# Kernel optimization log

Measured on AMD Instinct MI355X. Metric: run time of the kernel, lower is better.

The kernel has to match this reference:

```python
import jax, jax.numpy as jnp
import numpy as np

NEG_INF = -1e30


def setup_inputs() -> dict:
    key = jax.random.key(0)
    ks = jax.random.split(key, 8)
    B, N, I, O, H = 8, 1024, 64, 32, 4
    return {
        "x": jax.random.normal(ks[0], (B, N, I), dtype=jnp.float32),
        "adj": jax.random.randint(ks[1], (N, N), 0, 2, dtype=jnp.int32),
        "source_prior": jax.random.normal(ks[2], (B, N), dtype=jnp.float32),
        "beta": jax.random.normal(ks[3], (H,), dtype=jnp.float32),
        "weight": jax.random.normal(ks[4], (H, I, O), dtype=jnp.float32) * (1.0 / np.sqrt(I)),
        "attn_src": jax.random.normal(ks[5], (H, O), dtype=jnp.float32) * (1.0 / np.sqrt(O)),
        "attn_dst": jax.random.normal(ks[6], (H, O), dtype=jnp.float32) * (1.0 / np.sqrt(O)),
        "bias": jnp.zeros((H, O), dtype=jnp.float32),
    }


def reference(x, adj, source_prior, beta, weight, attn_src, attn_dst, bias):
    B, N, _ = x.shape
    H, _, O = weight.shape
    # Per-head projection + bias: [B,H,N,O]
    projected = jnp.einsum('bni,hio->bhno', x, weight) + bias[None, :, None, :]
    src_scores = jnp.einsum('bhnd,hd->bhn', projected, attn_src)  # [B,H,N]
    dst_scores = jnp.einsum('bhnd,hd->bhn', projected, attn_dst)  # [B,H,N]
    # Additive attention logits: [B,H,dst,src]
    logits = jax.nn.leaky_relu(dst_scores[..., :, None] + src_scores[..., None, :],
                               negative_slope=0.2)
    # Source-prior correction
    gain = jax.nn.softplus(beta).reshape(1, H, 1, 1)
    logits = logits + gain * source_prior[:, None, None, :]
    # Masked softmax over sources; fully-masked rows stay zero
    mask = (adj != 0)[None, None, :, :]  # [1,1,N,N]
    masked = jnp.where(mask, logits, NEG_INF)
    row_max = jnp.max(masked, axis=-1, keepdims=True)
    row_max = jnp.where(jnp.isfinite(row_max) & (row_max > NEG_INF / 2),
                        row_max, jnp.zeros_like(row_max))
    exp_logits = jnp.where(mask, jnp.exp(logits - row_max), 0.0)
    eps = jnp.finfo(logits.dtype).eps
    denom = jnp.maximum(jnp.sum(exp_logits, axis=-1, keepdims=True), eps)
    attention = exp_logits / denom  # [B,H,N,N]
    # Weighted aggregation: [B,H,N,O]
    output = jnp.einsum('bhij,bhjd->bhid', attention, projected)
    # concat=True: [B,N,H*O]
    encoded = jnp.transpose(output, (0, 2, 1, 3)).reshape(B, N, H * O)
    return encoded
```

## Files before the change

kernel.cpp:

```cpp
#include <hip/hip_runtime.h>
#include <math.h>

#define NB 8
#define NN 1024
#define NI 64
#define NO 32
#define NH 4
#define NEGINF (-1e30f)

typedef _Float16 half8 __attribute__((ext_vector_type(8)));
typedef _Float16 half4v __attribute__((ext_vector_type(4)));
typedef float floatx4 __attribute__((ext_vector_type(4)));

__global__ __launch_bounds__(256) void k_pack(const int* __restrict__ adj,
                                              unsigned char* __restrict__ adjb) {
    const int i = blockIdx.x * 256 + threadIdx.x;
    const int4 v = ((const int4*)adj)[i];
    unsigned int p = (v.x ? 1u : 0u) | ((v.y ? 1u : 0u) << 8) |
                     ((v.z ? 1u : 0u) << 16) | ((v.w ? 1u : 0u) << 24);
    ((unsigned int*)adjb)[i] = p;
}

__global__ __launch_bounds__(256) void k_proj(
    const float* __restrict__ x, const float* __restrict__ beta,
    const float* __restrict__ weight, const float* __restrict__ attn_src,
    const float* __restrict__ attn_dst, const float* __restrict__ bias,
    const float* __restrict__ prior,
    _Float16* __restrict__ projT,
    float* __restrict__ src_s, float* __restrict__ dst_s, float* __restrict__ gp)
{
    __shared__ __align__(16) float xs[32 * 64];
    __shared__ __align__(16) float ws[4 * 64 * 36];
    const int t = threadIdx.x;
    const int ntile = blockIdx.x, b = blockIdx.y;
    const int n0b = ntile * 32;
    {
        const float4* xsrc = (const float4*)(x + ((size_t)b * NN + n0b) * NI);
        float4* xd = (float4*)xs;
        xd[t] = xsrc[t];
        xd[t + 256] = xsrc[t + 256];
    }
    #pragma unroll
    for (int k = 0; k < 8; ++k) {
        int e = t + k * 256;
        int h = e >> 9, rem = e & 511, i = rem >> 3, o4 = rem & 7;
        float4 wv = *(const float4*)(weight + (h * NI + i) * NO + o4 * 4);
        *(float4*)&ws[h * 2304 + i * 36 + o4 * 4] = wv;
    }
    __syncthreads();

    const int o4 = t & 7, h = (t >> 3) & 3, ng = t >> 5;
    const int o0 = o4 * 4, nl0 = ng * 4;
    float acc[4][4];
    #pragma unroll
    for (int kn = 0; kn < 4; ++kn)
        #pragma unroll
        for (int oo = 0; oo < 4; ++oo) acc[kn][oo] = 0.f;

    for (int i = 0; i < NI; ++i) {
        const float4 wv = *(const float4*)&ws[h * 2304 + i * 36 + o0];
        #pragma unroll
        for (int kn = 0; kn < 4; ++kn) {
            const float xv = xs[(nl0 + kn) * 64 + i];
            acc[kn][0] = fmaf(xv, wv.x, acc[kn][0]);
            acc[kn][1] = fmaf(xv, wv.y, acc[kn][1]);
            acc[kn][2] = fmaf(xv, wv.z, acc[kn][2]);
            acc[kn][3] = fmaf(xv, wv.w, acc[kn][3]);
        }
    }
    const float4 bv  = *(const float4*)(bias + h * NO + o0);
    const float4 asv = *(const float4*)(attn_src + h * NO + o0);
    const float4 adv = *(const float4*)(attn_dst + h * NO + o0);
    const int bh = b * NH + h;
    float ssum[4], dsum[4];
    #pragma unroll
    for (int kn = 0; kn < 4; ++kn) {
        acc[kn][0] += bv.x; acc[kn][1] += bv.y;
        acc[kn][2] += bv.z; acc[kn][3] += bv.w;
        ssum[kn] = acc[kn][0]*asv.x + acc[kn][1]*asv.y + acc[kn][2]*asv.z + acc[kn][3]*asv.w;
        dsum[kn] = acc[kn][0]*adv.x + acc[kn][1]*adv.y + acc[kn][2]*adv.z + acc[kn][3]*adv.w;
    }
    #pragma unroll
    for (int oo = 0; oo < 4; ++oo) {
        half4v hv;
        hv[0] = (_Float16)acc[0][oo]; hv[1] = (_Float16)acc[1][oo];
        hv[2] = (_Float16)acc[2][oo]; hv[3] = (_Float16)acc[3][oo];
        *(half4v*)(projT + ((size_t)(bh * NO + o0 + oo)) * NN + n0b + nl0) = hv;
    }
    #pragma unroll
    for (int msk = 1; msk <= 4; msk <<= 1) {
        #pragma unroll
        for (int kn = 0; kn < 4; ++kn) {
            ssum[kn] += __shfl_xor(ssum[kn], msk, 64);
            dsum[kn] += __shfl_xor(dsum[kn], msk, 64);
        }
    }
    if (o4 == 0) {
        const float bx = beta[h];
        const float sp = fmaxf(bx, 0.f) + log1pf(__expf(-fabsf(bx)));
        #pragma unroll
        for (int kn = 0; kn < 4; ++kn) {
            const int n = n0b + nl0 + kn;
            src_s[bh * NN + n] = ssum[kn];
            dst_s[bh * NN + n] = dsum[kn];
            gp[bh * NN + n] = sp * prior[b * NN + n];
        }
    }
}

#define SPH 512
#define SP  520

__global__ __launch_bounds__(256) void k_attn(
    const unsigned char* __restrict__ adjb,
    const _Float16* __restrict__ projT,
    const float* __restrict__ src_s, const float* __restrict__ dst_s,
    const float* __restrict__ gp,
    float* __restrict__ out)
{
    __shared__ __align__(16) _Float16 vt[NO * SP];
    __shared__ __align__(16) float srcs[NN];
    __shared__ __align__(16) float gps[NN];
    const int t = threadIdx.x;
    const int lane = t & 63, wave = t >> 6;
    const int dtile = blockIdx.x, h = blockIdx.y, b = blockIdx.z;
    const int bh = b * NH + h;
    {
        ((float4*)srcs)[t] = ((const float4*)(src_s + bh * NN))[t];
        ((float4*)gps)[t]  = ((const float4*)(gp + bh * NN))[t];
    }
    const int m = lane & 15, quad = lane >> 4;
    const int d = dtile * 64 + wave * 16 + m;
    const float dreg = dst_s[bh * NN + d];
    const unsigned char* adjr = adjb + (size_t)d * NN;
    const _Float16* ptrow = projT + (size_t)bh * NO * NN;

    floatx4 acc0 = {0.f, 0.f, 0.f, 0.f}, acc1 = {0.f, 0.f, 0.f, 0.f};
    float m_s = NEGINF, l_s = 0.f;
    uint2 apre = *(const uint2*)(adjr + quad * 8);

    for (int ph = 0; ph < 2; ++ph) {
        #pragma unroll
        for (int rr = 0; rr < 8; ++rr) {
            const int o = wave * 8 + rr;
            *(half8*)&vt[o * SP + lane * 8] =
                *(const half8*)(ptrow + (size_t)o * NN + ph * SPH + lane * 8);
        }
        __syncthreads();
        for (int st = 0; st < 16; ++st) {
            const int gs = ph * 16 + st;
            const uint2 acur = apre;
            if (gs < 31) apre = *(const uint2*)(adjr + (gs + 1) * 32 + quad * 8);
            const int sg = gs * 32 + quad * 8;
            const float4 s_lo = *(const float4*)&srcs[sg];
            const float4 s_hi = *(const float4*)&srcs[sg + 4];
            const float4 g_lo = *(const float4*)&gps[sg];
            const float4 g_hi = *(const float4*)&gps[sg + 4];
            const float sv[8] = {s_lo.x, s_lo.y, s_lo.z, s_lo.w,
                                 s_hi.x, s_hi.y, s_hi.z, s_hi.w};
            const float gv[8] = {g_lo.x, g_lo.y, g_lo.z, g_lo.w,
                                 g_hi.x, g_hi.y, g_hi.z, g_hi.w};
            float scm[8], mkf[8];
            #pragma unroll
            for (int j = 0; j < 8; ++j) {
                const unsigned int bit =
                    ((j < 4 ? (acur.x >> (8 * j)) : (acur.y >> (8 * (j - 4)))) & 1u);
                const float ts = dreg + sv[j];
                const float lk = fmaxf(ts, 0.f) + 0.2f * fminf(ts, 0.f);
                const float sc = lk + gv[j];
                mkf[j] = bit ? 1.f : 0.f;
                scm[j] = bit ? sc : NEGINF;
            }
            float mq = scm[0];
            #pragma unroll
            for (int j = 1; j < 8; ++j) mq = fmaxf(mq, scm[j]);
            mq = fmaxf(mq, __shfl_xor(mq, 16, 64));
            mq = fmaxf(mq, __shfl_xor(mq, 32, 64));
            const float m_new = fmaxf(m_s, mq);
            const float alpha = __expf(m_s - m_new);
            m_s = m_new;
            float p[8], psum = 0.f;
            #pragma unroll
            for (int j = 0; j < 8; ++j) {
                p[j] = mkf[j] * __expf(scm[j] - m_new);
                psum += p[j];
            }
            psum += __shfl_xor(psum, 16, 64);
            psum += __shfl_xor(psum, 32, 64);
            l_s = l_s * alpha + psum;
            #pragma unroll
            for (int r = 0; r < 4; ++r) {
                const float ar = __shfl(alpha, quad * 4 + r, 64);
                acc0[r] *= ar; acc1[r] *= ar;
            }
            half8 af;
            #pragma unroll
            for (int j = 0; j < 8; ++j) af[j] = (_Float16)p[j];
            const int sl = st * 32 + quad * 8;
            const half8 b0 = *(const half8*)&vt[m * SP + sl];
            const half8 b1 = *(const half8*)&vt[(16 + m) * SP + sl];
            acc0 = __builtin_amdgcn_mfma_f32_16x16x32_f16(af, b0, acc0, 0, 0, 0);
            acc1 = __builtin_amdgcn_mfma_f32_16x16x32_f16(af, b1, acc1, 0, 0, 0);
        }
        __syncthreads();
    }
    #pragma unroll
    for (int r = 0; r < 4; ++r) {
        const int row = quad * 4 + r;
        const float lr = __shfl(l_s, row, 64);
        const float inv = 1.f / fmaxf(lr, 1.1920929e-07f);
        float* go = out + ((size_t)(b * NN + dtile * 64 + wave * 16 + row)) * (NH * NO) + h * NO;
        go[m] = acc0[r] * inv;
        go[16 + m] = acc1[r] * inv;
    }
}

extern "C" void kernel_launch(void* const* d_in, const int* in_sizes, int n_in,
                              void* d_out, int out_size, void* d_ws, size_t ws_size,
                              hipStream_t stream) {
    (void)in_sizes; (void)n_in; (void)out_size; (void)ws_size;
    const float* x        = (const float*)d_in[0];
    const int*   adj      = (const int*)d_in[1];
    const float* prior    = (const float*)d_in[2];
    const float* beta     = (const float*)d_in[3];
    const float* weight   = (const float*)d_in[4];
    const float* attn_src = (const float*)d_in[5];
    const float* attn_dst = (const float*)d_in[6];
    const float* bias     = (const float*)d_in[7];
    float* out = (float*)d_out;

    _Float16* projT = (_Float16*)d_ws;
    float* src_s = (float*)((char*)d_ws + (1 << 21));
    float* dst_s = src_s + NB * NH * NN;
    float* gpb   = dst_s + NB * NH * NN;
    unsigned char* adjb = (unsigned char*)(gpb + NB * NH * NN);

    hipLaunchKernelGGL(k_pack, dim3(1024), dim3(256), 0, stream, adj, adjb);
    hipLaunchKernelGGL(k_proj, dim3(32, 8), dim3(256), 0, stream,
                       x, beta, weight, attn_src, attn_dst, bias, prior,
                       projT, src_s, dst_s, gpb);
    hipLaunchKernelGGL(k_attn, dim3(16, 4, 8), dim3(256), 0, stream,
                       adjb, projT, src_s, dst_s, gpb, out);
}
```

Baseline: 103.6 us.

## Replace online softmax with two-pass max prepass and stage full V tile

The attention kernel first computes each destination row's exact max logit in a separate pass, with each of the four waves scanning a quarter of the sources and combining through shared memory. The main loop then computes exp against that fixed max, which removes the online-softmax rescaling: the per-step cross-lane max, the alpha exp and the accumulator shuffles. The whole 32x1024 half-precision V tile is now loaded into LDS once, replacing the two-phase load and its extra barriers. The cost is a second pass over the adjacency bits and logits plus more LDS per block, which may lower occupancy. A small unroll pragma is also added to the projection loop.

```diff
diff --git a/kernel.cpp b/kernel.cpp
--- a/kernel.cpp
+++ b/kernel.cpp
@@ -57,6 +57,7 @@
         #pragma unroll
         for (int oo = 0; oo < 4; ++oo) acc[kn][oo] = 0.f;
 
+    #pragma unroll 4
     for (int i = 0; i < NI; ++i) {
         const float4 wv = *(const float4*)&ws[h * 2304 + i * 36 + o0];
         #pragma unroll
@@ -108,8 +109,7 @@
     }
 }
 
-#define SPH 512
-#define SP  520
+#define VTP 1032
 
 __global__ __launch_bounds__(256) void k_attn(
     const unsigned char* __restrict__ adjb,
@@ -118,96 +118,100 @@
     const float* __restrict__ gp,
     float* __restrict__ out)
 {
-    __shared__ __align__(16) _Float16 vt[NO * SP];
+    __shared__ __align__(16) _Float16 vt[NO * VTP];
     __shared__ __align__(16) float srcs[NN];
     __shared__ __align__(16) float gps[NN];
+    __shared__ float pmax[64 * 4];
     const int t = threadIdx.x;
     const int lane = t & 63, wave = t >> 6;
     const int dtile = blockIdx.x, h = blockIdx.y, b = blockIdx.z;
     const int bh = b * NH + h;
+
+    ((float4*)srcs)[t] = ((const float4*)(src_s + bh * NN))[t];
+    ((float4*)gps)[t]  = ((const float4*)(gp + bh * NN))[t];
+    const _Float16* ptrow = projT + (size_t)bh * NO * NN;
+    #pragma unroll
+    for (int k = 0; k < 16; ++k) {
+        const int e = t + k * 256;
+        const int o = e >> 7, sc8 = e & 127;
+        *(half8*)&vt[o * VTP + sc8 * 8] =
+            *(const half8*)(ptrow + (size_t)o * NN + sc8 * 8);
+    }
+    __syncthreads();
+
     {
-        ((float4*)srcs)[t] = ((const float4*)(src_s + bh * NN))[t];
-        ((float4*)gps)[t]  = ((const float4*)(gp + bh * NN))[t];
-    }
+        const int dl = lane, qt = wave;
+        const int drow = dtile * 64 + dl;
+        const float dv = dst_s[bh * NN + drow];
+        const unsigned char* ar = adjb + (size_t)drow * NN + qt * 256;
+        float mx = NEGINF;
+        #pragma unroll 4
+        for (int k = 0; k < 16; ++k) {
+            const uint4 a4 = *(const uint4*)(ar + k * 16);
+            const unsigned int wv[4] = {a4.x, a4.y, a4.z, a4.w};
+            const int sb = qt * 256 + k * 16;
+            #pragma unroll
+            for (int w = 0; w < 4; ++w) {
+                #pragma unroll
+                for (int byi = 0; byi < 4; ++byi) {
+                    const int s = sb + w * 4 + byi;
+                    const float ts = dv + srcs[s];
+                    const float sc = fmaxf(ts, 0.f) + 0.2f * fminf(ts, 0.f) + gps[s];
+                    const bool on = (wv[w] >> (8 * byi)) & 1;
+                    mx = fmaxf(mx, on ? sc : NEGINF);
+                }
+            }
+        }
+        pmax[dl * 4 + qt] = mx;
+    }
+    __syncthreads();
+
     const int m = lane & 15, quad = lane >> 4;
     const int d = dtile * 64 + wave * 16 + m;
     const float dreg = dst_s[bh * NN + d];
+    const int pmb = (wave * 16 + m) * 4;
+    const float rmx = fmaxf(fmaxf(pmax[pmb], pmax[pmb + 1]),
+                            fmaxf(pmax[pmb + 2], pmax[pmb + 3]));
+    const float rmc = (rmx > -1e29f) ? rmx : 0.f;
     const unsigned char* adjr = adjb + (size_t)d * NN;
-    const _Float16* ptrow = projT + (size_t)bh * NO * NN;
 
     floatx4 acc0 = {0.f, 0.f, 0.f, 0.f}, acc1 = {0.f, 0.f, 0.f, 0.f};
-    float m_s = NEGINF, l_s = 0.f;
+    float psum = 0.f;
     uint2 apre = *(const uint2*)(adjr + quad * 8);
 
-    for (int ph = 0; ph < 2; ++ph) {
-        #pragma unroll
-        for (int rr = 0; rr < 8; ++rr) {
-            const int o = wave * 8 + rr;
-            *(half8*)&vt[o * SP + lane * 8] =
-                *(const half8*)(ptrow + (size_t)o * NN + ph * SPH + lane * 8);
-        }
-        __syncthreads();
-        for (int st = 0; st < 16; ++st) {
-            const int gs = ph * 16 + st;
-            const uint2 acur = apre;
-            if (gs < 31) apre = *(const uint2*)(adjr + (gs + 1) * 32 + quad * 8);
-            const int sg = gs * 32 + quad * 8;
-            const float4 s_lo = *(const float4*)&srcs[sg];
-            const float4 s_hi = *(const float4*)&srcs[sg + 4];
-            const float4 g_lo = *(const float4*)&gps[sg];
-            const float4 g_hi = *(const float4*)&gps[sg + 4];
-            const float sv[8] = {s_lo.x, s_lo.y, s_lo.z, s_lo.w,
-                                 s_hi.x, s_hi.y, s_hi.z, s_hi.w};
-            const float gv[8] = {g_lo.x, g_lo.y, g_lo.z, g_lo.w,
-                                 g_hi.x, g_hi.y, g_hi.z, g_hi.w};
-            float scm[8], mkf[8];
-            #pragma unroll
-            for (int j = 0; j < 8; ++j) {
-                const unsigned int bit =
-                    ((j < 4 ? (acur.x >> (8 * j)) : (acur.y >> (8 * (j - 4)))) & 1u);
-                const float ts = dreg + sv[j];
-                const float lk = fmaxf(ts, 0.f) + 0.2f * fminf(ts, 0.f);
-                const float sc = lk + gv[j];
-                mkf[j] = bit ? 1.f : 0.f;
-                scm[j] = bit ? sc : NEGINF;
-            }
-            float mq = scm[0];
-            #pragma unroll
-            for (int j = 1; j < 8; ++j) mq = fmaxf(mq, scm[j]);
-            mq = fmaxf(mq, __shfl_xor(mq, 16, 64));
-            mq = fmaxf(mq, __shfl_xor(mq, 32, 64));
-            const float m_new = fmaxf(m_s, mq);
-            const float alpha = __expf(m_s - m_new);
-            m_s = m_new;
-            float p[8], psum = 0.f;
-            #pragma unroll
-            for (int j = 0; j < 8; ++j) {
-                p[j] = mkf[j] * __expf(scm[j] - m_new);
-                psum += p[j];
-            }
-            psum += __shfl_xor(psum, 16, 64);
-            psum += __shfl_xor(psum, 32, 64);
-            l_s = l_s * alpha + psum;
-            #pragma unroll
-            for (int r = 0; r < 4; ++r) {
-                const float ar = __shfl(alpha, quad * 4 + r, 64);
-                acc0[r] *= ar; acc1[r] *= ar;
-            }
-            half8 af;
-            #pragma unroll
-            for (int j = 0; j < 8; ++j) af[j] = (_Float16)p[j];
-            const int sl = st * 32 + quad * 8;
-            const half8 b0 = *(const half8*)&vt[m * SP + sl];
-            const half8 b1 = *(const half8*)&vt[(16 + m) * SP + sl];
-            acc0 = __builtin_amdgcn_mfma_f32_16x16x32_f16(af, b0, acc0, 0, 0, 0);
-            acc1 = __builtin_amdgcn_mfma_f32_16x16x32_f16(af, b1, acc1, 0, 0, 0);
-        }
-        __syncthreads();
-    }
+    for (int st = 0; st < 32; ++st) {
+        const uint2 acur = apre;
+        if (st < 31) apre = *(const uint2*)(adjr + (st + 1) * 32 + quad * 8);
+        const int sg = st * 32 + quad * 8;
+        float sv[8], gv[8];
+        *(float4*)&sv[0] = *(const float4*)&srcs[sg];
+        *(float4*)&sv[4] = *(const float4*)&srcs[sg + 4];
+        *(float4*)&gv[0] = *(const float4*)&gps[sg];
+        *(float4*)&gv[4] = *(const float4*)&gps[sg + 4];
+        half8 af;
+        #pragma unroll
+        for (int j = 0; j < 8; ++j) {
+            const unsigned int bit =
+                ((j < 4 ? (acur.x >> (8 * j)) : (acur.y >> (8 * (j - 4)))) & 1u);
+            const float ts = dreg + sv[j];
+            const float lk = fmaxf(ts, 0.f) + 0.2f * fminf(ts, 0.f);
+            const float sce = bit ? (lk + gv[j]) : NEGINF;
+            const float p = __expf(sce - rmc);
+            psum += p;
+            af[j] = (_Float16)p;
+        }
+        const half8 b0 = *(const half8*)&vt[m * VTP + sg];
+        const half8 b1 = *(const half8*)&vt[(16 + m) * VTP + sg];
+        acc0 = __builtin_amdgcn_mfma_f32_16x16x32_f16(af, b0, acc0, 0, 0, 0);
+        acc1 = __builtin_amdgcn_mfma_f32_16x16x32_f16(af, b1, acc1, 0, 0, 0);
+    }
+    psum += __shfl_xor(psum, 16, 64);
+    psum += __shfl_xor(psum, 32, 64);
+
     #pragma unroll
     for (int r = 0; r < 4; ++r) {
         const int row = quad * 4 + r;
-        const float lr = __shfl(l_s, row, 64);
+        const float lr = __shfl(psum, row, 64);
         const float inv = 1.f / fmaxf(lr, 1.1920929e-07f);
         float* go = out + ((size_t)(b * NN + dtile * 64 + wave * 16 + row)) * (NH * NO) + h * NO;
         go[m] = acc0[r] * inv;
```

After: 110.0 us. 6.2% more time.
